# Kernel tuning notes

Hardware: AMD Instinct MI355X
Metric: run time of the kernel (lower is better)

## Reference

```python
import jax, jax.numpy as jnp
import numpy as np

B, S, D, H = 2, 2048, 1024, 16
DEPTH = D // H


def setup_inputs() -> dict:
    key = jax.random.key(0)
    ks = jax.random.split(key, 12)
    inp = {
        "q": jax.random.normal(ks[0], (B, S, D), jnp.float32),
        "k": jax.random.normal(ks[1], (B, S, D), jnp.float32),
        "v": jax.random.normal(ks[2], (B, S - 1, D), jnp.float32),
        # causal mask for the sliced (S-1, S-1) score grid: 1 where masked out
        "mask": jnp.broadcast_to(
            jnp.triu(jnp.ones((S - 1, S - 1), jnp.float32), k=1), (B, S - 1, S - 1)
        ),
        "Wq": jax.random.normal(ks[3], (D, D), jnp.float32) * 0.02,
        "bq": jnp.zeros((D,), jnp.float32),
        "Wk": jax.random.normal(ks[4], (D, D), jnp.float32) * 0.02,
        "bk": jnp.zeros((D,), jnp.float32),
        "Wv": jax.random.normal(ks[5], (D, D), jnp.float32) * 0.02,
        "bv": jnp.zeros((D,), jnp.float32),
        "Wo": jax.random.normal(ks[6], (D, D), jnp.float32) * 0.02,
        "bo": jnp.zeros((D,), jnp.float32),
    }
    return inp


def _split_heads(x):
    # (B, L, D) -> (B, H, L, depth)
    b, l, _ = x.shape
    return x.reshape(b, l, H, DEPTH).transpose(0, 2, 1, 3)


def reference(q, k, v, mask, Wq, bq, Wk, bk, Wv, bv, Wo, bo):
    qq = q @ Wq + bq            # q_layers[0]
    kk = k @ Wk + bk            # k_layers[0]
    vv = v @ Wv + bv            # wv
    qh, kh, vh = _split_heads(qq), _split_heads(kk), _split_heads(vv)
    # scores: (B, H, S, S) then sliced to (B, H, S-1, S-1) as in the source
    scores = jnp.einsum('bhqd,bhkd->bhqk', qh, kh)[:, :, 1:, :-1]
    scale = 1.0 / jnp.sqrt(jnp.asarray(DEPTH, jnp.float32))
    # original casts to fp64 here; JAX default x64-disabled => computed in fp32
    logits = scores * scale + mask[:, None, :, :] * (-1e9)
    att = jax.nn.softmax(logits, axis=-1)   # (B, H, S-1, S-1)
    ctx = jnp.einsum('bhqk,bhkd->bhqd', att, vh)  # v seq len is S-1
    ctx = ctx.transpose(0, 2, 1, 3).reshape(q.shape[0], -1, D)
    out = ctx @ Wo + bo
    return out, att
```

## Files before the change

kernel.cpp:

```cpp
#include <hip/hip_runtime.h>


typedef __attribute__((ext_vector_type(8))) short bf16x8;
typedef __attribute__((ext_vector_type(4))) float f32x4;

#define MFMA_BF16(A, B, C) __builtin_amdgcn_mfma_f32_16x16x32_bf16(A, B, C, 0, 0, 0)

__device__ __forceinline__ short f2bf(float x) {
    unsigned u = __float_as_uint(x);
    u = u + 0x7FFFu + ((u >> 16) & 1u);
    return (short)(u >> 16);
}
__device__ __forceinline__ float bf2f(short s) {
    return __uint_as_float(((unsigned)(unsigned short)s) << 16);
}
__device__ __forceinline__ int imin(int a, int b) { return a < b ? a : b; }

__device__ __forceinline__ float fexp2(float x) {
#if __has_builtin(__builtin_amdgcn_exp2f)
    return __builtin_amdgcn_exp2f(x);
#else
    return __expf(x * 0.69314718055994531f);
#endif
}

__device__ __forceinline__ void dma16(const short* g, short* l) {
    __builtin_amdgcn_global_load_lds(
        (const __attribute__((address_space(1))) unsigned int*)g,
        (__attribute__((address_space(3))) unsigned int*)l, 16, 0, 0);
}

__global__ __launch_bounds__(256) void transpose_split_kernel(
    const float* __restrict__ W, short* __restrict__ Thi, short* __restrict__ Tlo) {
    __shared__ float tile[32][33];
    const int tx = threadIdx.x & 31, ty = threadIdx.x >> 5;
    const int k0 = blockIdx.x * 32, n0 = blockIdx.y * 32;
#pragma unroll
    for (int p = 0; p < 4; ++p)
        tile[ty + p * 8][tx] = W[(size_t)(k0 + ty + p * 8) * 1024 + n0 + tx];
    __syncthreads();
#pragma unroll
    for (int p = 0; p < 4; ++p) {
        int n = n0 + ty + p * 8, k = k0 + tx;
        float x = tile[tx][ty + p * 8];
        short h = f2bf(x);
        Thi[(size_t)n * 1024 + k] = h;
        if (Tlo) Tlo[(size_t)n * 1024 + k] = f2bf(x - bf2f(h));
    }
}

__global__ __launch_bounds__(256) void split_kernel(
    const float* __restrict__ X, short* __restrict__ Hi, short* __restrict__ Lo, int n8) {
    int idx = blockIdx.x * 256 + threadIdx.x;
    if (idx >= n8) return;
    float4 x0 = *((const float4*)X + (size_t)idx * 2);
    float4 x1 = *((const float4*)X + (size_t)idx * 2 + 1);
    float xs[8] = {x0.x, x0.y, x0.z, x0.w, x1.x, x1.y, x1.z, x1.w};
    bf16x8 hv, lv;
#pragma unroll
    for (int e = 0; e < 8; ++e) {
        short h = f2bf(xs[e]);
        hv[e] = h;
        lv[e] = f2bf(xs[e] - bf2f(h));
    }
    *(bf16x8*)&Hi[(size_t)idx * 8] = hv;
    if (Lo) *(bf16x8*)&Lo[(size_t)idx * 8] = lv;
}

template <int SPLIT, int OUTMODE>
__global__ __launch_bounds__(256) void gemm_dma(
    const short* __restrict__ Ahg, const short* __restrict__ Alg, int M,
    const short* __restrict__ Bhg, const short* __restrict__ Blg,
    const float* __restrict__ bias, float scale,
    float* __restrict__ Cf, short* __restrict__ Chi, short* __restrict__ Clo) {
    __shared__ __align__(16) short Ah[512 * 8];
    __shared__ __align__(16) short Al[SPLIT ? 512 * 8 : 8];
    __shared__ __align__(16) short Bh[256 * 8];
    __shared__ __align__(16) short Bl[SPLIT ? 256 * 8 : 8];

    const int tid = threadIdx.x;
    const int w = tid >> 6, lane = tid & 63;
    const int quad = lane >> 4, l16 = lane & 15;
    const int m0 = blockIdx.y * 128, n0 = blockIdx.x * 64;
    const int row0 = (w & 1) * 64, col0 = (w >> 1) * 32;

    f32x4 acc[4][2];
#pragma unroll
    for (int mi = 0; mi < 4; ++mi)
#pragma unroll
        for (int ni = 0; ni < 2; ++ni) acc[mi][ni] = (f32x4){0.f, 0.f, 0.f, 0.f};

    const int a_row = tid & 127;
    const int a_gr = imin(m0 + a_row, M - 1);
    const int b_gr = n0 + (tid & 63);
    const int b_c = tid >> 6;

    for (int k0 = 0; k0 < 1024; k0 += 32) {
        __syncthreads();
#pragma unroll
        for (int p = 0; p < 2; ++p) {
            int c = (p * 256 + tid) >> 7;
            const size_t go = (size_t)a_gr * 1024 + k0 + c * 8;
            dma16(Ahg + go, &Ah[(p * 256 + tid) * 8]);
            if (SPLIT) dma16(Alg + go, &Al[(p * 256 + tid) * 8]);
        }
        {
            const size_t go = (size_t)b_gr * 1024 + k0 + b_c * 8;
            dma16(Bhg + go, &Bh[tid * 8]);
            if (SPLIT) dma16(Blg + go, &Bl[tid * 8]);
        }
        __syncthreads();

        bf16x8 af[4], afl[4], bfr[2], bfl[2];
#pragma unroll
        for (int mi = 0; mi < 4; ++mi) {
            int r = row0 + mi * 16 + l16;
            af[mi] = *(const bf16x8*)&Ah[(quad * 128 + r) * 8];
            if (SPLIT) afl[mi] = *(const bf16x8*)&Al[(quad * 128 + r) * 8];
        }
#pragma unroll
        for (int ni = 0; ni < 2; ++ni) {
            int cdx = col0 + ni * 16 + l16;
            bfr[ni] = *(const bf16x8*)&Bh[(quad * 64 + cdx) * 8];
            if (SPLIT) bfl[ni] = *(const bf16x8*)&Bl[(quad * 64 + cdx) * 8];
        }
#pragma unroll
        for (int mi = 0; mi < 4; ++mi)
#pragma unroll
            for (int ni = 0; ni < 2; ++ni) {
                acc[mi][ni] = MFMA_BF16(af[mi], bfr[ni], acc[mi][ni]);
                if (SPLIT) {
                    acc[mi][ni] = MFMA_BF16(af[mi], bfl[ni], acc[mi][ni]);
                    acc[mi][ni] = MFMA_BF16(afl[mi], bfr[ni], acc[mi][ni]);
                }
            }
    }

#pragma unroll
    for (int ni = 0; ni < 2; ++ni) {
        int col = n0 + col0 + ni * 16 + l16;
        float bv = bias[col];
#pragma unroll
        for (int mi = 0; mi < 4; ++mi) {
#pragma unroll
            for (int r = 0; r < 4; ++r) {
                int row = m0 + row0 + mi * 16 + quad * 4 + r;
                if (row < M) {
                    float c = (acc[mi][ni][r] + bv) * scale;
                    size_t off = (size_t)row * 1024 + col;
                    if (OUTMODE == 0) {
                        Cf[off] = c;
                    } else if (OUTMODE == 1) {
                        Chi[off] = f2bf(c);
                    } else {
                        short h = f2bf(c);
                        Chi[off] = h;
                        Clo[off] = f2bf(c - bf2f(h));
                    }
                }
            }
        }
    }
}

__global__ __launch_bounds__(256) void transpose_v_kernel(
    const short* __restrict__ VV, short* __restrict__ VT) {
    __shared__ short t[64][72];
    const int tid = threadIdx.x;
    const int st = blockIdx.x & 31, bh = blockIdx.x >> 5;
    const int b = bh >> 4, h = bh & 15;
    const int s0 = st * 64;
    {
        int seq = s0 + (tid >> 2), d0 = (tid & 3) * 16;
        int seqc = imin(seq, 2046);
        const short* src = VV + ((size_t)(b * 2047 + seqc)) * 1024 + h * 64 + d0;
        bf16x8 v0 = *(const bf16x8*)src;
        bf16x8 v1 = *(const bf16x8*)(src + 8);
        bool ok = (seq <= 2046);
#pragma unroll
        for (int e = 0; e < 8; ++e) {
            t[d0 + e][tid >> 2] = ok ? v0[e] : (short)0;
            t[d0 + 8 + e][tid >> 2] = ok ? v1[e] : (short)0;
        }
    }
    __syncthreads();
    {
        int d = tid >> 2, sc2 = (tid & 3) * 16;
        bf16x8 o0, o1;
#pragma unroll
        for (int e = 0; e < 8; ++e) {
            o0[e] = t[d][sc2 + e];
            o1[e] = t[d][sc2 + 8 + e];
        }
        short* dst = VT + ((size_t)(bh * 64 + d)) * 2048 + s0 + sc2;
        *(bf16x8*)dst = o0;
        *(bf16x8*)(dst + 8) = o1;
    }
}

__global__ __launch_bounds__(256) void attn_kernel(
    const short* __restrict__ QQh, const short* __restrict__ QQl,
    const short* __restrict__ KKh, const short* __restrict__ KKl,
    const short* __restrict__ VT,
    float* __restrict__ att, short* __restrict__ CTX) {
    __shared__ __align__(16) short KH[2][512 * 8];
    __shared__ __align__(16) short KL[2][512 * 8];
    __shared__ __align__(16) short VS[2][512 * 8];
    __shared__ __align__(16) short Ps[4][16 * 72];

    const int tid = threadIdx.x;
    const int w = tid >> 6, lane = tid & 63;
    const int quad = lane >> 4, l16 = lane & 15;
    const int bx = blockIdx.x;
    const int qt = 31 - (bx >> 5);
    const int bh = bx & 31;
    const int h = bh & 15, b = bh >> 4;
    const int i0 = qt * 64;

    const int i_frag = i0 + w * 16 + l16;
    const int qrow = imin(i_frag + 1, 2047);
    const size_t qoff = ((size_t)(b * 2048 + qrow)) * 1024 + h * 64;
    const bf16x8 qh0 = *(const bf16x8*)&QQh[qoff + 0 + quad * 8];
    const bf16x8 qh1 = *(const bf16x8*)&QQh[qoff + 32 + quad * 8];
    const bf16x8 ql0 = *(const bf16x8*)&QQl[qoff + 0 + quad * 8];
    const bf16x8 ql1 = *(const bf16x8*)&QQl[qoff + 32 + quad * 8];

    const int i_max = imin(i0 + 63, 2046);
    const int jt_max = i_max >> 6;
    const int wave_imax = imin(i0 + w * 16 + 15, 2046);
    const int rowbase = i0 + w * 16 + quad * 4;

    const int dma_key = tid & 63;
    const int dma_cc0 = tid >> 6;

    float lsum[4] = {0.f, 0.f, 0.f, 0.f};

    auto stageA = [&](int jt, int buf) {
#pragma unroll
        for (int p = 0; p < 2; ++p) {
            int cc = p * 4 + dma_cc0;
            dma16(KKh + ((size_t)(b * 2048 + jt * 64 + dma_key)) * 1024 + h * 64 + cc * 8,
                  &KH[buf][(p * 256 + tid) * 8]);
        }
    };
    auto stageB = [&](int jt, int buf) {
#pragma unroll
        for (int p = 0; p < 2; ++p) {
            int cc = p * 4 + dma_cc0;
            const size_t ko =
                ((size_t)(b * 2048 + jt * 64 + dma_key)) * 1024 + h * 64 + cc * 8;
            dma16(KKh + ko, &KH[buf][(p * 256 + tid) * 8]);
            dma16(KKl + ko, &KL[buf][(p * 256 + tid) * 8]);
            dma16(VT + ((size_t)(bh * 64 + dma_key)) * 2048 + jt * 64 + cc * 8,
                  &VS[buf][(p * 256 + tid) * 8]);
        }
    };

    stageA(0, 0);
    __syncthreads();
    int cur = 0;
    for (int jt = 0; jt <= jt_max; ++jt) {
        if (jt < jt_max) stageA(jt + 1, cur ^ 1);
        const int j0 = jt * 64;
        if (j0 <= wave_imax) {
#pragma unroll
            for (int s = 0; s < 4; ++s) {
                f32x4 sc = (f32x4){0.f, 0.f, 0.f, 0.f};
#pragma unroll
                for (int c = 0; c < 2; ++c) {
                    bf16x8 kh =
                        *(const bf16x8*)&KH[cur][((c * 4 + quad) * 64 + s * 16 + l16) * 8];
                    sc = MFMA_BF16(c ? qh1 : qh0, kh, sc);
                    sc = MFMA_BF16(c ? ql1 : ql0, kh, sc);
                }
                int j = j0 + s * 16 + l16;
#pragma unroll
                for (int r = 0; r < 4; ++r) {
                    int i = rowbase + r;
                    if (j <= i && i <= 2046) lsum[r] += fexp2(sc[r]);
                }
            }
        }
        __syncthreads();
        cur ^= 1;
    }
#pragma unroll
    for (int m = 1; m < 16; m <<= 1) {
#pragma unroll
        for (int r = 0; r < 4; ++r) lsum[r] += __shfl_xor(lsum[r], m, 64);
    }
    float linv[4];
#pragma unroll
    for (int r = 0; r < 4; ++r) linv[r] = 1.0f / lsum[r];

    f32x4 cacc[4];
#pragma unroll
    for (int t = 0; t < 4; ++t) cacc[t] = (f32x4){0.f, 0.f, 0.f, 0.f};

    stageB(0, 0);
    __syncthreads();
    cur = 0;
    for (int jt = 0; jt <= jt_max; ++jt) {
        if (jt < jt_max) stageB(jt + 1, cur ^ 1);
        const int j0 = jt * 64;
        if (j0 <= wave_imax) {
#pragma unroll
            for (int s = 0; s < 4; ++s) {
                f32x4 sc = (f32x4){0.f, 0.f, 0.f, 0.f};
#pragma unroll
                for (int c = 0; c < 2; ++c) {
                    const int ci = ((c * 4 + quad) * 64 + s * 16 + l16) * 8;
                    bf16x8 kh = *(const bf16x8*)&KH[cur][ci];
                    bf16x8 kl = *(const bf16x8*)&KL[cur][ci];
                    bf16x8 ah = c ? qh1 : qh0;
                    bf16x8 al = c ? ql1 : ql0;
                    sc = MFMA_BF16(ah, kh, sc);
                    sc = MFMA_BF16(ah, kl, sc);
                    sc = MFMA_BF16(al, kh, sc);
                }
                int j = j0 + s * 16 + l16;
#pragma unroll
                for (int r = 0; r < 4; ++r) {
                    int i = rowbase + r;
                    bool valid = (j <= i) && (i <= 2046);
                    float p = valid ? fexp2(sc[r]) * linv[r] : 0.0f;
                    if (i <= 2046 && j <= 2046)
                        att[((size_t)bh * 2047 + i) * 2047 + j] = p;
                    Ps[w][(quad * 4 + r) * 72 + s * 16 + l16] = f2bf(p);
                }
            }
#pragma unroll
            for (int c = 0; c < 2; ++c) {
                bf16x8 pa = *(const bf16x8*)&Ps[w][l16 * 72 + c * 32 + quad * 8];
#pragma unroll
                for (int t = 0; t < 4; ++t) {
                    bf16x8 vb =
                        *(const bf16x8*)&VS[cur][((c * 4 + quad) * 64 + t * 16 + l16) * 8];
                    cacc[t] = MFMA_BF16(pa, vb, cacc[t]);
                }
            }
        } else {
#pragma unroll
            for (int s = 0; s < 4; ++s) {
                int j = j0 + s * 16 + l16;
#pragma unroll
                for (int r = 0; r < 4; ++r) {
                    int i = rowbase + r;
                    if (i <= 2046 && j <= 2046)
                        att[((size_t)bh * 2047 + i) * 2047 + j] = 0.0f;
                }
            }
        }
        __syncthreads();
        cur ^= 1;
    }

#pragma unroll
    for (int t = 0; t < 4; ++t) {
#pragma unroll
        for (int r = 0; r < 4; ++r) {
            int i = rowbase + r;
            if (i <= 2046)
                CTX[((size_t)(b * 2047 + i)) * 1024 + h * 64 + t * 16 + l16] = f2bf(cacc[t][r]);
        }
    }

    const int js = (jt_max + 1) * 64;
    if (js < 2047) {
        const float4 z4 = {0.f, 0.f, 0.f, 0.f};
        for (int i = i0; i <= i_max; ++i) {
            const size_t base = (size_t)(bh * 2047 + i) * 2047;
            float* rowp = att + base;
            int aligned = js + (int)((4 - ((base + js) & 3)) & 3);
            if (aligned > 2047) aligned = 2047;
            for (int c = js + tid; c < aligned; c += 256) rowp[c] = 0.0f;
            int nv = (2047 - aligned) >> 2;
            for (int q = tid; q < nv; q += 256)
                *(float4*)(rowp + aligned + q * 4) = z4;
            for (int c = aligned + nv * 4 + tid; c < 2047; c += 256) rowp[c] = 0.0f;
        }
    }
}

extern "C" void kernel_launch(void* const* d_in, const int* in_sizes, int n_in,
                              void* d_out, int out_size, void* d_ws, size_t ws_size,
                              hipStream_t stream) {
    (void)in_sizes; (void)n_in; (void)out_size; (void)ws_size;
    const float* q  = (const float*)d_in[0];
    const float* k  = (const float*)d_in[1];
    const float* v  = (const float*)d_in[2];
    const float* Wq = (const float*)d_in[4];
    const float* bq = (const float*)d_in[5];
    const float* Wk = (const float*)d_in[6];
    const float* bk = (const float*)d_in[7];
    const float* Wv = (const float*)d_in[8];
    const float* bv = (const float*)d_in[9];
    const float* Wo = (const float*)d_in[10];
    const float* bo = (const float*)d_in[11];

    float* out = (float*)d_out;
    float* att = out + (size_t)2 * 2047 * 1024;

    char* ws = (char*)d_ws;
    size_t off = 0;
    auto alloc = [&](size_t bytes) -> void* {
        void* p = ws + off;
        off += (bytes + 255) & ~(size_t)255;
        return p;
    };
    short* Wqt_h = (short*)alloc((size_t)1024 * 1024 * 2);
    short* Wqt_l = (short*)alloc((size_t)1024 * 1024 * 2);
    short* Wkt_h = (short*)alloc((size_t)1024 * 1024 * 2);
    short* Wkt_l = (short*)alloc((size_t)1024 * 1024 * 2);
    short* Wvt_h = (short*)alloc((size_t)1024 * 1024 * 2);
    short* Wot_h = (short*)alloc((size_t)1024 * 1024 * 2);
    short* Qhi = (short*)alloc((size_t)4096 * 1024 * 2);
    short* Qlo = (short*)alloc((size_t)4096 * 1024 * 2);
    short* Khi = (short*)alloc((size_t)4096 * 1024 * 2);
    short* Klo = (short*)alloc((size_t)4096 * 1024 * 2);
    short* Vbf = (short*)alloc((size_t)4096 * 1024 * 2);
    short* QQh = (short*)alloc((size_t)4096 * 1024 * 2);
    short* QQl = (short*)alloc((size_t)4096 * 1024 * 2);
    short* KKh = (short*)alloc((size_t)4096 * 1024 * 2);
    short* KKl = (short*)alloc((size_t)4096 * 1024 * 2);
    short* VV  = (short*)alloc((size_t)4096 * 1024 * 2);
    short* VT  = (short*)alloc((size_t)2048 * 2048 * 2 * 2);
    short* CTX = (short*)alloc((size_t)4096 * 1024 * 2);

    dim3 tgrid(32, 32);
    transpose_split_kernel<<<tgrid, 256, 0, stream>>>(Wq, Wqt_h, Wqt_l);
    transpose_split_kernel<<<tgrid, 256, 0, stream>>>(Wk, Wkt_h, Wkt_l);
    transpose_split_kernel<<<tgrid, 256, 0, stream>>>(Wv, Wvt_h, nullptr);
    transpose_split_kernel<<<tgrid, 256, 0, stream>>>(Wo, Wot_h, nullptr);

    split_kernel<<<2048, 256, 0, stream>>>(q, Qhi, Qlo, 4096 * 1024 / 8);
    split_kernel<<<2048, 256, 0, stream>>>(k, Khi, Klo, 4096 * 1024 / 8);
    split_kernel<<<2047, 256, 0, stream>>>(v, Vbf, nullptr, 4094 * 1024 / 8);

    dim3 ggrid(16, 32);
    const float qscale = 0.125f * 1.44269504088896341f;
    gemm_dma<1, 2><<<ggrid, 256, 0, stream>>>(Qhi, Qlo, 4096, Wqt_h, Wqt_l, bq, qscale,
                                              nullptr, QQh, QQl);
    gemm_dma<1, 2><<<ggrid, 256, 0, stream>>>(Khi, Klo, 4096, Wkt_h, Wkt_l, bk, 1.0f,
                                              nullptr, KKh, KKl);
    gemm_dma<0, 1><<<ggrid, 256, 0, stream>>>(Vbf, nullptr, 4094, Wvt_h, nullptr, bv, 1.0f,
                                              nullptr, VV, nullptr);

    transpose_v_kernel<<<dim3(32 * 32), 256, 0, stream>>>(VV, VT);

    attn_kernel<<<dim3(32 * 32), 256, 0, stream>>>(QQh, QQl, KKh, KKl, VT, att, CTX);

    gemm_dma<0, 0><<<ggrid, 256, 0, stream>>>(CTX, nullptr, 4094, Wot_h, nullptr, bo, 1.0f,
                                              out, nullptr, nullptr);
}
```

Before: 988.5 us.

## Load K/V fragments directly from global memory and merge QKV projections into one launch

The attention kernel drops its double-buffered LDS staging of K, K-low and V^T, along with the block barriers. Each wave now reads its MFMA fragments straight from global memory and only loops over its own causal range. The Q/K/V projection GEMMs are merged into one launch with a z-dimension selector, the output GEMM gets its own kernel, and both load the B (weight) operand directly from global memory into registers instead of through LDS. This removes shared-memory traffic, barriers and launch overhead. The cost is global loads that no longer coalesce well and are repeated across waves, now relying on L1/L2 caching, and the runtime-selected split path adds branches.

```diff
diff --git a/kernel.cpp b/kernel.cpp
--- a/kernel.cpp
+++ b/kernel.cpp
@@ -67,16 +67,32 @@
     if (Lo) *(bf16x8*)&Lo[(size_t)idx * 8] = lv;
 }
 
-template <int SPLIT, int OUTMODE>
-__global__ __launch_bounds__(256) void gemm_dma(
-    const short* __restrict__ Ahg, const short* __restrict__ Alg, int M,
-    const short* __restrict__ Bhg, const short* __restrict__ Blg,
-    const float* __restrict__ bias, float scale,
-    float* __restrict__ Cf, short* __restrict__ Chi, short* __restrict__ Clo) {
+__global__ __launch_bounds__(256) void gemm_qkv(
+    const short* __restrict__ Qhi, const short* __restrict__ Qlo,
+    const short* __restrict__ Khi, const short* __restrict__ Klo,
+    const short* __restrict__ Vbf,
+    const short* __restrict__ Wqh, const short* __restrict__ Wql,
+    const short* __restrict__ Wkh, const short* __restrict__ Wkl,
+    const short* __restrict__ Wvh,
+    const float* __restrict__ bq, const float* __restrict__ bk,
+    const float* __restrict__ bv, float qscale,
+    short* __restrict__ QQh, short* __restrict__ QQl,
+    short* __restrict__ KKh, short* __restrict__ KKl,
+    short* __restrict__ VVo) {
     __shared__ __align__(16) short Ah[512 * 8];
-    __shared__ __align__(16) short Al[SPLIT ? 512 * 8 : 8];
-    __shared__ __align__(16) short Bh[256 * 8];
-    __shared__ __align__(16) short Bl[SPLIT ? 256 * 8 : 8];
+    __shared__ __align__(16) short Al[512 * 8];
+
+    const int z = blockIdx.z;
+    const bool split = (z < 2);
+    const short* Ahg = (z == 0) ? Qhi : ((z == 1) ? Khi : Vbf);
+    const short* Alg = (z == 0) ? Qlo : Klo;
+    const short* Bhg = (z == 0) ? Wqh : ((z == 1) ? Wkh : Wvh);
+    const short* Blg = (z == 0) ? Wql : Wkl;
+    const float* bias = (z == 0) ? bq : ((z == 1) ? bk : bv);
+    const float scale = (z == 0) ? qscale : 1.0f;
+    const int M = (z == 2) ? 4094 : 4096;
+    short* Chi = (z == 0) ? QQh : ((z == 1) ? KKh : VVo);
+    short* Clo = (z == 0) ? QQl : KKl;
 
     const int tid = threadIdx.x;
     const int w = tid >> 6, lane = tid & 63;
@@ -90,48 +106,42 @@
 #pragma unroll
         for (int ni = 0; ni < 2; ++ni) acc[mi][ni] = (f32x4){0.f, 0.f, 0.f, 0.f};
 
-    const int a_row = tid & 127;
-    const int a_gr = imin(m0 + a_row, M - 1);
-    const int b_gr = n0 + (tid & 63);
-    const int b_c = tid >> 6;
+    const int a_gr = imin(m0 + (tid & 127), M - 1);
 
     for (int k0 = 0; k0 < 1024; k0 += 32) {
         __syncthreads();
 #pragma unroll
         for (int p = 0; p < 2; ++p) {
-            int c = (p * 256 + tid) >> 7;
+            int idx = p * 256 + tid;
+            int c = idx >> 7;
             const size_t go = (size_t)a_gr * 1024 + k0 + c * 8;
-            dma16(Ahg + go, &Ah[(p * 256 + tid) * 8]);
-            if (SPLIT) dma16(Alg + go, &Al[(p * 256 + tid) * 8]);
-        }
-        {
-            const size_t go = (size_t)b_gr * 1024 + k0 + b_c * 8;
-            dma16(Bhg + go, &Bh[tid * 8]);
-            if (SPLIT) dma16(Blg + go, &Bl[tid * 8]);
+            dma16(Ahg + go, &Ah[idx * 8]);
+            if (split) dma16(Alg + go, &Al[idx * 8]);
+        }
+        bf16x8 bfh[2], bfl[2];
+#pragma unroll
+        for (int ni = 0; ni < 2; ++ni) {
+            const size_t bo = (size_t)(n0 + col0 + ni * 16 + l16) * 1024 + k0 + quad * 8;
+            bfh[ni] = *(const bf16x8*)&Bhg[bo];
+            if (split) bfl[ni] = *(const bf16x8*)&Blg[bo];
         }
         __syncthreads();
 
-        bf16x8 af[4], afl[4], bfr[2], bfl[2];
+        bf16x8 af[4], afl[4];
 #pragma unroll
         for (int mi = 0; mi < 4; ++mi) {
             int r = row0 + mi * 16 + l16;
             af[mi] = *(const bf16x8*)&Ah[(quad * 128 + r) * 8];
-            if (SPLIT) afl[mi] = *(const bf16x8*)&Al[(quad * 128 + r) * 8];
-        }
-#pragma unroll
-        for (int ni = 0; ni < 2; ++ni) {
-            int cdx = col0 + ni * 16 + l16;
-            bfr[ni] = *(const bf16x8*)&Bh[(quad * 64 + cdx) * 8];
-            if (SPLIT) bfl[ni] = *(const bf16x8*)&Bl[(quad * 64 + cdx) * 8];
+            if (split) afl[mi] = *(const bf16x8*)&Al[(quad * 128 + r) * 8];
         }
 #pragma unroll
         for (int mi = 0; mi < 4; ++mi)
 #pragma unroll
             for (int ni = 0; ni < 2; ++ni) {
-                acc[mi][ni] = MFMA_BF16(af[mi], bfr[ni], acc[mi][ni]);
-                if (SPLIT) {
+                acc[mi][ni] = MFMA_BF16(af[mi], bfh[ni], acc[mi][ni]);
+                if (split) {
                     acc[mi][ni] = MFMA_BF16(af[mi], bfl[ni], acc[mi][ni]);
-                    acc[mi][ni] = MFMA_BF16(afl[mi], bfr[ni], acc[mi][ni]);
+                    acc[mi][ni] = MFMA_BF16(afl[mi], bfh[ni], acc[mi][ni]);
                 }
             }
     }
@@ -139,27 +149,81 @@
 #pragma unroll
     for (int ni = 0; ni < 2; ++ni) {
         int col = n0 + col0 + ni * 16 + l16;
-        float bv = bias[col];
+        float bv_ = bias[col];
 #pragma unroll
         for (int mi = 0; mi < 4; ++mi) {
 #pragma unroll
             for (int r = 0; r < 4; ++r) {
                 int row = m0 + row0 + mi * 16 + quad * 4 + r;
                 if (row < M) {
-                    float c = (acc[mi][ni][r] + bv) * scale;
+                    float c = (acc[mi][ni][r] + bv_) * scale;
                     size_t off = (size_t)row * 1024 + col;
-                    if (OUTMODE == 0) {
-                        Cf[off] = c;
-                    } else if (OUTMODE == 1) {
-                        Chi[off] = f2bf(c);
-                    } else {
-                        short h = f2bf(c);
-                        Chi[off] = h;
-                        Clo[off] = f2bf(c - bf2f(h));
-                    }
-                }
-            }
-        }
+                    short hsv = f2bf(c);
+                    Chi[off] = hsv;
+                    if (split) Clo[off] = f2bf(c - bf2f(hsv));
+                }
+            }
+        }
+    }
+}
+
+__global__ __launch_bounds__(256) void gemm_o(
+    const short* __restrict__ Ahg, int M, const short* __restrict__ Bhg,
+    const float* __restrict__ bias, float* __restrict__ Cf) {
+    __shared__ __align__(16) short Ah[512 * 8];
+
+    const int tid = threadIdx.x;
+    const int w = tid >> 6, lane = tid & 63;
+    const int quad = lane >> 4, l16 = lane & 15;
+    const int m0 = blockIdx.y * 128, n0 = blockIdx.x * 64;
+    const int row0 = (w & 1) * 64, col0 = (w >> 1) * 32;
+
+    f32x4 acc[4][2];
+#pragma unroll
+    for (int mi = 0; mi < 4; ++mi)
+#pragma unroll
+        for (int ni = 0; ni < 2; ++ni) acc[mi][ni] = (f32x4){0.f, 0.f, 0.f, 0.f};
+
+    const int a_gr = imin(m0 + (tid & 127), M - 1);
+
+    for (int k0 = 0; k0 < 1024; k0 += 32) {
+        __syncthreads();
+#pragma unroll
+        for (int p = 0; p < 2; ++p) {
+            int idx = p * 256 + tid;
+            int c = idx >> 7;
+            dma16(Ahg + (size_t)a_gr * 1024 + k0 + c * 8, &Ah[idx * 8]);
+        }
+        bf16x8 bfh[2];
+#pragma unroll
+        for (int ni = 0; ni < 2; ++ni) {
+            const size_t bo = (size_t)(n0 + col0 + ni * 16 + l16) * 1024 + k0 + quad * 8;
+            bfh[ni] = *(const bf16x8*)&Bhg[bo];
+        }
+        __syncthreads();
+
+        bf16x8 af[4];
+#pragma unroll
+        for (int mi = 0; mi < 4; ++mi)
+            af[mi] = *(const bf16x8*)&Ah[(quad * 128 + row0 + mi * 16 + l16) * 8];
+#pragma unroll
+        for (int mi = 0; mi < 4; ++mi)
+#pragma unroll
+            for (int ni = 0; ni < 2; ++ni)
+                acc[mi][ni] = MFMA_BF16(af[mi], bfh[ni], acc[mi][ni]);
+    }
+
+#pragma unroll
+    for (int ni = 0; ni < 2; ++ni) {
+        int col = n0 + col0 + ni * 16 + l16;
+        float bv_ = bias[col];
+#pragma unroll
+        for (int mi = 0; mi < 4; ++mi)
+#pragma unroll
+            for (int r = 0; r < 4; ++r) {
+                int row = m0 + row0 + mi * 16 + quad * 4 + r;
+                if (row < M) Cf[(size_t)row * 1024 + col] = acc[mi][ni][r] + bv_;
+            }
     }
 }
 
@@ -203,9 +267,6 @@
     const short* __restrict__ KKh, const short* __restrict__ KKl,
     const short* __restrict__ VT,
     float* __restrict__ att, short* __restrict__ CTX) {
-    __shared__ __align__(16) short KH[2][512 * 8];
-    __shared__ __align__(16) short KL[2][512 * 8];
-    __shared__ __align__(16) short VS[2][512 * 8];
     __shared__ __align__(16) short Ps[4][16 * 72];
 
     const int tid = threadIdx.x;
@@ -228,90 +289,58 @@
     const int i_max = imin(i0 + 63, 2046);
     const int jt_max = i_max >> 6;
     const int wave_imax = imin(i0 + w * 16 + 15, 2046);
+    const int wave_jtmax = wave_imax >> 6;
     const int rowbase = i0 + w * 16 + quad * 4;
 
-    const int dma_key = tid & 63;
-    const int dma_cc0 = tid >> 6;
+    const size_t kbase = ((size_t)(b * 2048 + l16)) * 1024 + h * 64 + quad * 8;
+    const size_t vbase = ((size_t)(bh * 64 + l16)) * 2048 + quad * 8;
 
     float lsum[4] = {0.f, 0.f, 0.f, 0.f};
 
-    auto stageA = [&](int jt, int buf) {
-#pragma unroll
-        for (int p = 0; p < 2; ++p) {
-            int cc = p * 4 + dma_cc0;
-            dma16(KKh + ((size_t)(b * 2048 + jt * 64 + dma_key)) * 1024 + h * 64 + cc * 8,
-                  &KH[buf][(p * 256 + tid) * 8]);
-        }
-    };
-    auto stageB = [&](int jt, int buf) {
-#pragma unroll
-        for (int p = 0; p < 2; ++p) {
-            int cc = p * 4 + dma_cc0;
-            const size_t ko =
-                ((size_t)(b * 2048 + jt * 64 + dma_key)) * 1024 + h * 64 + cc * 8;
-            dma16(KKh + ko, &KH[buf][(p * 256 + tid) * 8]);
-            dma16(KKl + ko, &KL[buf][(p * 256 + tid) * 8]);
-            dma16(VT + ((size_t)(bh * 64 + dma_key)) * 2048 + jt * 64 + cc * 8,
-                  &VS[buf][(p * 256 + tid) * 8]);
-        }
-    };
-
-    stageA(0, 0);
-    __syncthreads();
-    int cur = 0;
+    for (int jt = 0; jt <= wave_jtmax; ++jt) {
+        const int j0 = jt * 64;
+#pragma unroll
+        for (int s = 0; s < 4; ++s) {
+            f32x4 sc = (f32x4){0.f, 0.f, 0.f, 0.f};
+            const size_t kr = kbase + (size_t)(j0 + s * 16) * 1024;
+#pragma unroll
+            for (int c = 0; c < 2; ++c) {
+                bf16x8 kh = *(const bf16x8*)&KKh[kr + c * 32];
+                sc = MFMA_BF16(c ? qh1 : qh0, kh, sc);
+                sc = MFMA_BF16(c ? ql1 : ql0, kh, sc);
+            }
+            int j = j0 + s * 16 + l16;
+#pragma unroll
+            for (int r = 0; r < 4; ++r) {
+                int i = rowbase + r;
+                if (j <= i && i <= 2046) lsum[r] += fexp2(sc[r]);
+            }
+        }
+    }
+#pragma unroll
+    for (int m = 1; m < 16; m <<= 1) {
+#pragma unroll
+        for (int r = 0; r < 4; ++r) lsum[r] += __shfl_xor(lsum[r], m, 64);
+    }
+    float linv[4];
+#pragma unroll
+    for (int r = 0; r < 4; ++r) linv[r] = 1.0f / lsum[r];
+
+    f32x4 cacc[4];
+#pragma unroll
+    for (int t = 0; t < 4; ++t) cacc[t] = (f32x4){0.f, 0.f, 0.f, 0.f};
+
     for (int jt = 0; jt <= jt_max; ++jt) {
-        if (jt < jt_max) stageA(jt + 1, cur ^ 1);
         const int j0 = jt * 64;
-        if (j0 <= wave_imax) {
+        if (jt <= wave_jtmax) {
 #pragma unroll
             for (int s = 0; s < 4; ++s) {
                 f32x4 sc = (f32x4){0.f, 0.f, 0.f, 0.f};
+                const size_t kr = kbase + (size_t)(j0 + s * 16) * 1024;
 #pragma unroll
                 for (int c = 0; c < 2; ++c) {
-                    bf16x8 kh =
-                        *(const bf16x8*)&KH[cur][((c * 4 + quad) * 64 + s * 16 + l16) * 8];
-                    sc = MFMA_BF16(c ? qh1 : qh0, kh, sc);
-                    sc = MFMA_BF16(c ? ql1 : ql0, kh, sc);
-                }
-                int j = j0 + s * 16 + l16;
-#pragma unroll
-                for (int r = 0; r < 4; ++r) {
-                    int i = rowbase + r;
-                    if (j <= i && i <= 2046) lsum[r] += fexp2(sc[r]);
-                }
-            }
-        }
-        __syncthreads();
-        cur ^= 1;
-    }
-#pragma unroll
-    for (int m = 1; m < 16; m <<= 1) {
-#pragma unroll
-        for (int r = 0; r < 4; ++r) lsum[r] += __shfl_xor(lsum[r], m, 64);
-    }
-    float linv[4];
-#pragma unroll
-    for (int r = 0; r < 4; ++r) linv[r] = 1.0f / lsum[r];
-
-    f32x4 cacc[4];
-#pragma unroll
-    for (int t = 0; t < 4; ++t) cacc[t] = (f32x4){0.f, 0.f, 0.f, 0.f};
-
-    stageB(0, 0);
-    __syncthreads();
-    cur = 0;
-    for (int jt = 0; jt <= jt_max; ++jt) {
-        if (jt < jt_max) stageB(jt + 1, cur ^ 1);
-        const int j0 = jt * 64;
-        if (j0 <= wave_imax) {
-#pragma unroll
-            for (int s = 0; s < 4; ++s) {
-                f32x4 sc = (f32x4){0.f, 0.f, 0.f, 0.f};
-#pragma unroll
-                for (int c = 0; c < 2; ++c) {
-                    const int ci = ((c * 4 + quad) * 64 + s * 16 + l16) * 8;
-                    bf16x8 kh = *(const bf16x8*)&KH[cur][ci];
-                    bf16x8 kl = *(const bf16x8*)&KL[cur][ci];
+                    bf16x8 kh = *(const bf16x8*)&KKh[kr + c * 32];
+                    bf16x8 kl = *(const bf16x8*)&KKl[kr + c * 32];
                     bf16x8 ah = c ? qh1 : qh0;
                     bf16x8 al = c ? ql1 : ql0;
                     sc = MFMA_BF16(ah, kh, sc);
@@ -334,8 +363,8 @@
                 bf16x8 pa = *(const bf16x8*)&Ps[w][l16 * 72 + c * 32 + quad * 8];
 #pragma unroll
                 for (int t = 0; t < 4; ++t) {
-                    bf16x8 vb =
-                        *(const bf16x8*)&VS[cur][((c * 4 + quad) * 64 + t * 16 + l16) * 8];
+                    bf16x8 vb = *(const bf16x8*)&VT[vbase + (size_t)t * 16 * 2048 +
+                                                    j0 + c * 32];
                     cacc[t] = MFMA_BF16(pa, vb, cacc[t]);
                 }
             }
@@ -351,8 +380,6 @@
                 }
             }
         }
-        __syncthreads();
-        cur ^= 1;
     }
 
 #pragma unroll
@@ -437,19 +464,14 @@
     split_kernel<<<2048, 256, 0, stream>>>(k, Khi, Klo, 4096 * 1024 / 8);
     split_kernel<<<2047, 256, 0, stream>>>(v, Vbf, nullptr, 4094 * 1024 / 8);
 
-    dim3 ggrid(16, 32);
     const float qscale = 0.125f * 1.44269504088896341f;
-    gemm_dma<1, 2><<<ggrid, 256, 0, stream>>>(Qhi, Qlo, 4096, Wqt_h, Wqt_l, bq, qscale,
-                                              nullptr, QQh, QQl);
-    gemm_dma<1, 2><<<ggrid, 256, 0, stream>>>(Khi, Klo, 4096, Wkt_h, Wkt_l, bk, 1.0f,
-                                              nullptr, KKh, KKl);
-    gemm_dma<0, 1><<<ggrid, 256, 0, stream>>>(Vbf, nullptr, 4094, Wvt_h, nullptr, bv, 1.0f,
-                                              nullptr, VV, nullptr);
+    gemm_qkv<<<dim3(16, 32, 3), 256, 0, stream>>>(
+        Qhi, Qlo, Khi, Klo, Vbf, Wqt_h, Wqt_l, Wkt_h, Wkt_l, Wvt_h,
+        bq, bk, bv, qscale, QQh, QQl, KKh, KKl, VV);
 
     transpose_v_kernel<<<dim3(32 * 32), 256, 0, stream>>>(VV, VT);
 
     attn_kernel<<<dim3(32 * 32), 256, 0, stream>>>(QQh, QQl, KKh, KKl, VT, att, CTX);
 
-    gemm_dma<0, 0><<<ggrid, 256, 0, stream>>>(CTX, nullptr, 4094, Wot_h, nullptr, bo, 1.0f,
-                                              out, nullptr, nullptr);
-}
+    gemm_o<<<dim3(16, 32), 256, 0, stream>>>(CTX, 4094, Wot_h, bo, out);
+}
```

After: 1.143 ms. 15.6% more time.
